# Optimization experiments

Hardware: AMD Instinct MI355X
Metric: run time of the kernel (lower is better)

Reference implementation:

```python
import jax, jax.numpy as jnp
import numpy as np

N_NODES, N_EDGES = 100000, 400000
D_NODE, D_EDGE, N_COND, N_ROUNDS = 128, 64, 2, 3


def gru_cell(x, h, Wih, Whh, bih, bhh):
    # Standard torch.nn.GRUCell math. x: [N, D] input, h: [N, D] hidden.
    gi = x @ Wih.T + bih            # [N, 3D]
    gh = h @ Whh.T + bhh            # [N, 3D]
    ir, iz, inn = jnp.split(gi, 3, axis=-1)
    hr, hz, hn = jnp.split(gh, 3, axis=-1)
    r = jax.nn.sigmoid(ir + hr)
    z = jax.nn.sigmoid(iz + hz)
    n = jnp.tanh(inn + r * hn)
    return (1.0 - z) * n + z * h


def setup_inputs() -> dict:
    key = jax.random.key(0)
    ks = jax.random.split(key, 10)
    scale = jnp.float32(0.05)
    d_in = 2 * D_NODE + D_EDGE + N_COND  # 322, matches enc_U Linear in_features
    h = jax.random.normal(ks[0], (N_NODES, D_NODE), jnp.float32)
    e = jax.random.normal(ks[1], (N_EDGES, D_EDGE), jnp.float32)
    src = jax.random.randint(ks[2], (N_EDGES,), 0, N_NODES)
    dst = jax.random.randint(ks[3], (N_EDGES,), 0, N_NODES)
    cond = jax.random.normal(ks[4], (N_COND,), jnp.float32)
    U_W = jax.random.normal(ks[5], (N_ROUNDS, D_NODE, d_in), jnp.float32) * scale
    U_b = jnp.zeros((N_ROUNDS, D_NODE), jnp.float32)
    Wih = jax.random.normal(ks[6], (N_ROUNDS, 3 * D_NODE, D_NODE), jnp.float32) * scale
    Whh = jax.random.normal(ks[7], (N_ROUNDS, 3 * D_NODE, D_NODE), jnp.float32) * scale
    bih = jnp.zeros((N_ROUNDS, 3 * D_NODE), jnp.float32)
    bhh = jnp.zeros((N_ROUNDS, 3 * D_NODE), jnp.float32)
    return dict(h=h, e=e, src=src, dst=dst, cond=cond,
                U_W=U_W, U_b=U_b, Wih=Wih, Whh=Whh, bih=bih, bhh=bhh)


def reference(h, e, src, dst, cond, U_W, U_b, Wih, Whh, bih, bhh):
    # GGM encode(): 3 rounds of gather-concat-Linear(enc_U)-segment_sum-GRUCell(enc_C).
    n_nodes = h.shape[0]
    n_edges = e.shape[0]
    cond_e = jnp.broadcast_to(cond, (n_edges, cond.shape[0]))
    for k in range(U_W.shape[0]):
        # per-edge message input: [h_v, h_w, e_vw, condition] -> [E, 2D+DE+NC]
        x = jnp.concatenate([h[dst], h[src], e, cond_e], axis=-1)
        msg = x @ U_W[k].T + U_b[k]                              # [E, D]
        agg = jax.ops.segment_sum(msg, dst, num_segments=n_nodes)  # [N, D]
        h = gru_cell(agg, h, Wih[k], Whh[k], bih[k], bhh[k])
    return h
```

## Files before the change

kernel.cpp:

```cpp
#include <hip/hip_runtime.h>
#include <hip/hip_bf16.h>
#include <hip/hip_fp16.h>


#define D_NODE 128
#define D_EDGE 64
#define D_IN   322
#define GRU3   384
#define ROWS_BLK 128
#define PA_STRIDE 328
#define PB_STRIDE 136

typedef _Float16 f16x8 __attribute__((ext_vector_type(8)));
typedef _Float16 f16x4 __attribute__((ext_vector_type(4)));
typedef _Float16 f16x2 __attribute__((ext_vector_type(2)));
typedef float    f32x4 __attribute__((ext_vector_type(4)));
typedef unsigned short u16x8 __attribute__((ext_vector_type(8)));

__device__ __forceinline__ f16x8 as_f16x8(u16x8 v) { return __builtin_bit_cast(f16x8, v); }
__device__ __forceinline__ float sigm_(float x) { return 1.f / (1.f + __expf(-x)); }
__device__ __forceinline__ float tanh_(float x) { return 1.f - 2.f / (__expf(2.f * x) + 1.f); }

__global__ void hist_k(const int* __restrict__ dst, int* __restrict__ cnt, int E) {
    int t = blockIdx.x * 256 + threadIdx.x;
    if (t < E) atomicAdd(&cnt[dst[t]], 1);
}

__global__ __launch_bounds__(256) void scan1_k(const int* __restrict__ cnt, int* __restrict__ row_ptr,
                                               int* __restrict__ blk_sums, int N) {
    __shared__ int s[256];
    const int t = threadIdx.x;
    const int base = blockIdx.x * 1024 + t * 4;
    int v0 = (base + 0 < N) ? cnt[base + 0] : 0;
    int v1 = (base + 1 < N) ? cnt[base + 1] : 0;
    int v2 = (base + 2 < N) ? cnt[base + 2] : 0;
    int v3 = (base + 3 < N) ? cnt[base + 3] : 0;
    const int tot = v0 + v1 + v2 + v3;
    s[t] = tot;
    __syncthreads();
    for (int off = 1; off < 256; off <<= 1) {
        int u = (t >= off) ? s[t - off] : 0;
        __syncthreads();
        s[t] += u;
        __syncthreads();
    }
    const int excl = s[t] - tot;
    if (base + 0 < N) row_ptr[base + 0] = excl;
    if (base + 1 < N) row_ptr[base + 1] = excl + v0;
    if (base + 2 < N) row_ptr[base + 2] = excl + v0 + v1;
    if (base + 3 < N) row_ptr[base + 3] = excl + v0 + v1 + v2;
    if (t == 255) blk_sums[blockIdx.x] = s[255];
}

__global__ __launch_bounds__(256) void scan2_k(int* __restrict__ blk_sums, int NB,
                                               int* __restrict__ row_ptr, int N, int E) {
    __shared__ int s[256];
    const int t = threadIdx.x;
    const int v = (t < NB) ? blk_sums[t] : 0;
    s[t] = v;
    __syncthreads();
    for (int off = 1; off < 256; off <<= 1) {
        int u = (t >= off) ? s[t - off] : 0;
        __syncthreads();
        s[t] += u;
        __syncthreads();
    }
    if (t < NB) blk_sums[t] = s[t] - v;
    if (t == 0) row_ptr[N] = E;
}

__global__ __launch_bounds__(256) void scan3_k(int* __restrict__ row_ptr, int* __restrict__ cursor,
                                               const int* __restrict__ blk_sums, int N) {
    const int off = blk_sums[blockIdx.x];
    const int base = blockIdx.x * 1024 + threadIdx.x * 4;
#pragma unroll
    for (int j = 0; j < 4; ++j) {
        const int i = base + j;
        if (i < N) {
            const int v = row_ptr[i] + off;
            row_ptr[i] = v;
            cursor[i] = v;
        }
    }
}

__global__ void scatter_k(const int* __restrict__ src, const int* __restrict__ dst,
                          int* __restrict__ cursor, int* __restrict__ csr_src,
                          int* __restrict__ csr_eid, int E) {
    int t = blockIdx.x * 256 + threadIdx.x;
    if (t < E) {
        int d = dst[t];
        int pos = atomicAdd(&cursor[d], 1);
        csr_src[pos] = src[t];
        csr_eid[pos] = t;
    }
}

__global__ __launch_bounds__(320) void cvt_uwp_k(const float* __restrict__ in, _Float16* __restrict__ out) {
    const int row = blockIdx.x;
    const int t = threadIdx.x;
    out[(size_t)row * 320 + t] = (_Float16)in[(size_t)row * D_IN + t];
}

__global__ void cvt_f32_k(const float* __restrict__ in, _Float16* __restrict__ out, int n) {
    int t = blockIdx.x * 256 + threadIdx.x;
    if (t < n) out[t] = (_Float16)in[t];
}

__global__ void cvt4_k(const float* __restrict__ in, _Float16* __restrict__ out, int n4) {
    int t = blockIdx.x * 256 + threadIdx.x;
    if (t < n4) {
        const f32x4 v = ((const f32x4*)in)[t];
        f16x4 r;
        r[0] = (_Float16)v[0]; r[1] = (_Float16)v[1];
        r[2] = (_Float16)v[2]; r[3] = (_Float16)v[3];
        ((f16x4*)out)[t] = r;
    }
}

__global__ void compute_c_k(const float* __restrict__ UW, const float* __restrict__ Ub,
                            const float* __restrict__ cond, float* __restrict__ cvec) {
    int t = threadIdx.x;
    if (t < 3 * D_NODE) {
        int k = t >> 7, i = t & 127;
        const float* u = UW + (size_t)k * D_NODE * D_IN + (size_t)i * D_IN + 320;
        cvec[t] = u[0] * cond[0] + u[1] * cond[1] + Ub[k * D_NODE + i];
    }
}

__global__ __launch_bounds__(256) void gather_e_k(const float* __restrict__ e,
                                                  const int* __restrict__ row_ptr,
                                                  const int* __restrict__ csr_eid,
                                                  _Float16* __restrict__ S_e, int N) {
    const int wave = threadIdx.x >> 6, lane = threadIdx.x & 63;
    const int n = blockIdx.x * 4 + wave;
    if (n >= N) return;
    const int p0 = row_ptr[n], p1 = row_ptr[n + 1];
    float a = 0.f, b = 0.f;
    int p = p0;
    for (; p + 1 < p1; p += 2) {
        const int e0 = csr_eid[p], e1 = csr_eid[p + 1];
        a += e[(size_t)e0 * D_EDGE + lane];
        b += e[(size_t)e1 * D_EDGE + lane];
    }
    if (p < p1) a += e[(size_t)csr_eid[p] * D_EDGE + lane];
    S_e[(size_t)n * D_EDGE + lane] = (_Float16)(a + b);
}

__global__ __launch_bounds__(256) void gather_h_k(const _Float16* __restrict__ h16,
                                                  const int* __restrict__ row_ptr,
                                                  const int* __restrict__ csr_src,
                                                  _Float16* __restrict__ S_h, int N) {
    const int wave = threadIdx.x >> 6, lane = threadIdx.x & 63;
    const int n = blockIdx.x * 4 + wave;
    if (n >= N) return;
    const unsigned* hp = (const unsigned*)h16;
    const int p0 = row_ptr[n], p1 = row_ptr[n + 1];
    float a0 = 0.f, a1 = 0.f, b0 = 0.f, b1 = 0.f;
    int p = p0;
    for (; p + 1 < p1; p += 2) {
        const int s0 = csr_src[p], s1 = csr_src[p + 1];
        const f16x2 v0 = __builtin_bit_cast(f16x2, hp[(size_t)s0 * 64 + lane]);
        const f16x2 v1 = __builtin_bit_cast(f16x2, hp[(size_t)s1 * 64 + lane]);
        a0 += (float)v0[0]; a1 += (float)v0[1];
        b0 += (float)v1[0]; b1 += (float)v1[1];
    }
    if (p < p1) {
        const f16x2 v = __builtin_bit_cast(f16x2, hp[(size_t)csr_src[p] * 64 + lane]);
        a0 += (float)v[0]; a1 += (float)v[1];
    }
    f16x2 r;
    r[0] = (_Float16)(a0 + b0);
    r[1] = (_Float16)(a1 + b1);
    ((unsigned*)S_h)[(size_t)n * 64 + lane] = __builtin_bit_cast(unsigned, r);
}

__global__ __launch_bounds__(256) void agg_k(
    const _Float16* __restrict__ h16,
    const _Float16* __restrict__ S_h,
    const _Float16* __restrict__ S_e,
    const int* __restrict__ row_ptr,
    const float* __restrict__ cvec,
    const _Float16* __restrict__ UWp,
    _Float16* __restrict__ agg,
    int N) {
    __shared__ __align__(16) _Float16 pbuf[2][16 * PA_STRIDE];

    const int tid  = threadIdx.x;
    const int wave = tid >> 6;
    const int lane = tid & 63;
    const int l15  = lane & 15;
    const int lg   = lane >> 4;
    const int rbase = blockIdx.x * ROWS_BLK + wave * 32;

    const unsigned short* hp  = (const unsigned short*)h16;
    const unsigned short* shp = (const unsigned short*)S_h;
    const unsigned short* sep = (const unsigned short*)S_e;
    const unsigned short* uwp = (const unsigned short*)UWp;

    f16x8 a_h[2][4], a_sh[2][4], a_se[2][2];
#pragma unroll
    for (int m = 0; m < 2; ++m) {
        const int arow = min(rbase + m * 16 + l15, N - 1);
#pragma unroll
        for (int kb = 0; kb < 4; ++kb) {
            a_h[m][kb]  = as_f16x8(*(const u16x8*)(hp  + (size_t)arow * D_NODE + kb * 32 + lg * 8));
            a_sh[m][kb] = as_f16x8(*(const u16x8*)(shp + (size_t)arow * D_NODE + kb * 32 + lg * 8));
        }
#pragma unroll
        for (int kb = 0; kb < 2; ++kb)
            a_se[m][kb] = as_f16x8(*(const u16x8*)(sep + (size_t)arow * D_EDGE + kb * 32 + lg * 8));
    }
    float degv[2][4];
#pragma unroll
    for (int m = 0; m < 2; ++m)
#pragma unroll
        for (int i = 0; i < 4; ++i) {
            const int n = min(rbase + m * 16 + lg * 4 + i, N - 1);
            degv[m][i] = (float)(row_ptr[n + 1] - row_ptr[n]);
        }

    u16x8 pr0, pr1, pr2;
    auto load_panel = [&](int nb) {
        const int c0 = tid, c1 = 256 + tid, c2 = 512 + tid;
        pr0 = *(const u16x8*)(uwp + (size_t)(nb * 16 + c0 / 40) * 320 + (c0 % 40) * 8);
        pr1 = *(const u16x8*)(uwp + (size_t)(nb * 16 + c1 / 40) * 320 + (c1 % 40) * 8);
        if (c2 < 640)
            pr2 = *(const u16x8*)(uwp + (size_t)(nb * 16 + c2 / 40) * 320 + (c2 % 40) * 8);
    };
    auto write_panel = [&](int b) {
        const int c0 = tid, c1 = 256 + tid, c2 = 512 + tid;
        *(u16x8*)&pbuf[b][(c0 / 40) * PA_STRIDE + (c0 % 40) * 8] = pr0;
        *(u16x8*)&pbuf[b][(c1 / 40) * PA_STRIDE + (c1 % 40) * 8] = pr1;
        if (c2 < 640)
            *(u16x8*)&pbuf[b][(c2 / 40) * PA_STRIDE + (c2 % 40) * 8] = pr2;
    };

    load_panel(0);
    write_panel(0);
    __syncthreads();

#pragma unroll 1
    for (int nb = 0; nb < 8; ++nb) {
        if (nb < 7) load_panel(nb + 1);
        const _Float16* bp = pbuf[nb & 1];
        f32x4 acc1[2] = {{0.f,0.f,0.f,0.f},{0.f,0.f,0.f,0.f}};
        f32x4 acc2[2] = {{0.f,0.f,0.f,0.f},{0.f,0.f,0.f,0.f}};
#pragma unroll
        for (int kb = 0; kb < 10; ++kb) {
            f16x8 b = as_f16x8(*(const u16x8*)&bp[l15 * PA_STRIDE + kb * 32 + lg * 8]);
            if (kb < 4) {
                acc1[0] = __builtin_amdgcn_mfma_f32_16x16x32_f16(a_h[0][kb], b, acc1[0], 0, 0, 0);
                acc1[1] = __builtin_amdgcn_mfma_f32_16x16x32_f16(a_h[1][kb], b, acc1[1], 0, 0, 0);
            } else if (kb < 8) {
                acc2[0] = __builtin_amdgcn_mfma_f32_16x16x32_f16(a_sh[0][kb-4], b, acc2[0], 0, 0, 0);
                acc2[1] = __builtin_amdgcn_mfma_f32_16x16x32_f16(a_sh[1][kb-4], b, acc2[1], 0, 0, 0);
            } else {
                acc2[0] = __builtin_amdgcn_mfma_f32_16x16x32_f16(a_se[0][kb-8], b, acc2[0], 0, 0, 0);
                acc2[1] = __builtin_amdgcn_mfma_f32_16x16x32_f16(a_se[1][kb-8], b, acc2[1], 0, 0, 0);
            }
        }
        const float cv = cvec[nb * 16 + l15];
#pragma unroll
        for (int m = 0; m < 2; ++m)
#pragma unroll
            for (int i = 0; i < 4; ++i) {
                const int n = rbase + m * 16 + lg * 4 + i;
                if (n < N)
                    agg[(size_t)n * D_NODE + nb * 16 + l15] =
                        (_Float16)(degv[m][i] * (acc1[m][i] + cv) + acc2[m][i]);
            }
        if (nb < 7) write_panel((nb + 1) & 1);
        __syncthreads();
    }
}

__global__ __launch_bounds__(256) void gru_k(
    const float* __restrict__ h_cur,
    _Float16* __restrict__ h16,
    const _Float16* __restrict__ agg,
    const _Float16* __restrict__ Wihh,
    const _Float16* __restrict__ Whhh,
    const float* __restrict__ bih,
    const float* __restrict__ bhh,
    float* __restrict__ h_next,
    int N) {
    __shared__ __align__(16) _Float16 pbuf[2][96 * PB_STRIDE];

    const int tid  = threadIdx.x;
    const int wave = tid >> 6;
    const int lane = tid & 63;
    const int l15  = lane & 15;
    const int lg   = lane >> 4;
    const int rbase = blockIdx.x * ROWS_BLK + wave * 32;

    const unsigned short* hp  = (const unsigned short*)h16;
    const unsigned short* agp = (const unsigned short*)agg;
    const unsigned short* wih = (const unsigned short*)Wihh;
    const unsigned short* whh = (const unsigned short*)Whhh;

    f16x8 a_ag[2][4], a_h[2][4];
#pragma unroll
    for (int m = 0; m < 2; ++m) {
        const int arow = min(rbase + m * 16 + l15, N - 1);
#pragma unroll
        for (int kb = 0; kb < 4; ++kb) {
            a_ag[m][kb] = as_f16x8(*(const u16x8*)(agp + (size_t)arow * D_NODE + kb * 32 + lg * 8));
            a_h[m][kb]  = as_f16x8(*(const u16x8*)(hp  + (size_t)arow * D_NODE + kb * 32 + lg * 8));
        }
    }

    u16x8 pr[6];
    auto load_panel = [&](int nb) {
#pragma unroll
        for (int r = 0; r < 6; ++r) {
            const int c = r * 256 + tid;
            const int row = c >> 4;
            const int off = (c & 15) * 8;
            const int gate = row >> 4;
            const int col = nb * 16 + (row & 15) + (gate % 3) * D_NODE;
            const unsigned short* mat = (gate < 3) ? wih : whh;
            pr[r] = *(const u16x8*)(mat + (size_t)col * D_NODE + off);
        }
    };
    auto write_panel = [&](int b) {
#pragma unroll
        for (int r = 0; r < 6; ++r) {
            const int c = r * 256 + tid;
            const int row = c >> 4;
            const int off = (c & 15) * 8;
            *(u16x8*)&pbuf[b][row * PB_STRIDE + off] = pr[r];
        }
    };

    load_panel(0);
    write_panel(0);
    __syncthreads();

#pragma unroll 1
    for (int nb = 0; nb < 8; ++nb) {
        if (nb < 7) load_panel(nb + 1);
        const int d = nb * 16 + l15;
        float hv[2][4];
#pragma unroll
        for (int m = 0; m < 2; ++m)
#pragma unroll
            for (int i = 0; i < 4; ++i) {
                const int n = min(rbase + m * 16 + lg * 4 + i, N - 1);
                hv[m][i] = h_cur[(size_t)n * D_NODE + d];
            }
        const float bir = bih[d],       biz = bih[128 + d], bin = bih[256 + d];
        const float bhr = bhh[d],       bhz = bhh[128 + d], bhn = bhh[256 + d];

        const _Float16* bp = pbuf[nb & 1];
        f32x4 air[2] = {{0.f,0.f,0.f,0.f},{0.f,0.f,0.f,0.f}};
        f32x4 aiz[2] = {{0.f,0.f,0.f,0.f},{0.f,0.f,0.f,0.f}};
        f32x4 ain_[2] = {{0.f,0.f,0.f,0.f},{0.f,0.f,0.f,0.f}};
        f32x4 ahr[2] = {{0.f,0.f,0.f,0.f},{0.f,0.f,0.f,0.f}};
        f32x4 ahz[2] = {{0.f,0.f,0.f,0.f},{0.f,0.f,0.f,0.f}};
        f32x4 ahn[2] = {{0.f,0.f,0.f,0.f},{0.f,0.f,0.f,0.f}};
#pragma unroll
        for (int kb = 0; kb < 4; ++kb) {
            const int ko = kb * 32 + lg * 8;
            f16x8 b;
            b = as_f16x8(*(const u16x8*)&bp[(0 * 16 + l15) * PB_STRIDE + ko]);
            air[0] = __builtin_amdgcn_mfma_f32_16x16x32_f16(a_ag[0][kb], b, air[0], 0, 0, 0);
            air[1] = __builtin_amdgcn_mfma_f32_16x16x32_f16(a_ag[1][kb], b, air[1], 0, 0, 0);
            b = as_f16x8(*(const u16x8*)&bp[(1 * 16 + l15) * PB_STRIDE + ko]);
            aiz[0] = __builtin_amdgcn_mfma_f32_16x16x32_f16(a_ag[0][kb], b, aiz[0], 0, 0, 0);
            aiz[1] = __builtin_amdgcn_mfma_f32_16x16x32_f16(a_ag[1][kb], b, aiz[1], 0, 0, 0);
            b = as_f16x8(*(const u16x8*)&bp[(2 * 16 + l15) * PB_STRIDE + ko]);
            ain_[0] = __builtin_amdgcn_mfma_f32_16x16x32_f16(a_ag[0][kb], b, ain_[0], 0, 0, 0);
            ain_[1] = __builtin_amdgcn_mfma_f32_16x16x32_f16(a_ag[1][kb], b, ain_[1], 0, 0, 0);
            b = as_f16x8(*(const u16x8*)&bp[(3 * 16 + l15) * PB_STRIDE + ko]);
            ahr[0] = __builtin_amdgcn_mfma_f32_16x16x32_f16(a_h[0][kb], b, ahr[0], 0, 0, 0);
            ahr[1] = __builtin_amdgcn_mfma_f32_16x16x32_f16(a_h[1][kb], b, ahr[1], 0, 0, 0);
            b = as_f16x8(*(const u16x8*)&bp[(4 * 16 + l15) * PB_STRIDE + ko]);
            ahz[0] = __builtin_amdgcn_mfma_f32_16x16x32_f16(a_h[0][kb], b, ahz[0], 0, 0, 0);
            ahz[1] = __builtin_amdgcn_mfma_f32_16x16x32_f16(a_h[1][kb], b, ahz[1], 0, 0, 0);
            b = as_f16x8(*(const u16x8*)&bp[(5 * 16 + l15) * PB_STRIDE + ko]);
            ahn[0] = __builtin_amdgcn_mfma_f32_16x16x32_f16(a_h[0][kb], b, ahn[0], 0, 0, 0);
            ahn[1] = __builtin_amdgcn_mfma_f32_16x16x32_f16(a_h[1][kb], b, ahn[1], 0, 0, 0);
        }
#pragma unroll
        for (int m = 0; m < 2; ++m)
#pragma unroll
            for (int i = 0; i < 4; ++i) {
                const int n = rbase + m * 16 + lg * 4 + i;
                if (n < N) {
                    const float r  = sigm_(air[m][i] + bir + ahr[m][i] + bhr);
                    const float z  = sigm_(aiz[m][i] + biz + ahz[m][i] + bhz);
                    const float nn = tanh_(ain_[m][i] + bin + r * (ahn[m][i] + bhn));
                    const float hval = (1.f - z) * nn + z * hv[m][i];
                    h_next[(size_t)n * D_NODE + d] = hval;
                    h16[(size_t)n * D_NODE + d] = (_Float16)hval;
                }
            }
        if (nb < 7) write_panel((nb + 1) & 1);
        __syncthreads();
    }
}

extern "C" void kernel_launch(void* const* d_in, const int* in_sizes, int n_in,
                              void* d_out, int out_size, void* d_ws, size_t ws_size,
                              hipStream_t stream) {
    const float* h0   = (const float*)d_in[0];
    const float* e    = (const float*)d_in[1];
    const int*   src  = (const int*)d_in[2];
    const int*   dst  = (const int*)d_in[3];
    const float* cond = (const float*)d_in[4];
    const float* UW   = (const float*)d_in[5];
    const float* Ub   = (const float*)d_in[6];
    const float* Wih  = (const float*)d_in[7];
    const float* Whh  = (const float*)d_in[8];
    const float* bih  = (const float*)d_in[9];
    const float* bhh  = (const float*)d_in[10];

    const int N = in_sizes[0] / D_NODE;
    const int E = in_sizes[2];
    const int NB = (N + 1023) / 1024;
    const int NT = (N + ROWS_BLK - 1) / ROWS_BLK;

    char* wsb = (char*)d_ws;
    size_t off = 0;
    auto carve = [&](size_t bytes) -> char* {
        char* p = wsb + off;
        off = (off + bytes + 255) & ~(size_t)255;
        return p;
    };
    int*   cnt      = (int*)carve((size_t)N * 4);
    int*   row_ptr  = (int*)carve(((size_t)N + 1) * 4);
    int*   cursor   = (int*)carve((size_t)N * 4);
    int*   csr_src  = (int*)carve((size_t)E * 4);
    int*   csr_eid  = (int*)carve((size_t)E * 4);
    int*   blk_sums = (int*)carve(256 * 4);
    float* cvec     = (float*)carve(3 * D_NODE * 4);
    _Float16* S_e  = (_Float16*)carve((size_t)N * D_EDGE * 2);
    _Float16* S_h  = (_Float16*)carve((size_t)N * D_NODE * 2);
    _Float16* aggb = (_Float16*)carve((size_t)N * D_NODE * 2);
    _Float16* h16  = (_Float16*)carve((size_t)N * D_NODE * 2);
    _Float16* UWp  = (_Float16*)carve((size_t)3 * D_NODE * 320 * 2);
    _Float16* Wihh = (_Float16*)carve((size_t)3 * GRU3 * D_NODE * 2);
    _Float16* Whhh = (_Float16*)carve((size_t)3 * GRU3 * D_NODE * 2);
    (void)ws_size; (void)n_in; (void)out_size;

    hipMemsetAsync(cnt, 0, (size_t)N * 4, stream);
    hist_k<<<(E + 255) / 256, 256, 0, stream>>>(dst, cnt, E);
    scan1_k<<<NB, 256, 0, stream>>>(cnt, row_ptr, blk_sums, N);
    scan2_k<<<1, 256, 0, stream>>>(blk_sums, NB, row_ptr, N, E);
    scan3_k<<<NB, 256, 0, stream>>>(row_ptr, cursor, blk_sums, N);
    scatter_k<<<(E + 255) / 256, 256, 0, stream>>>(src, dst, cursor, csr_src, csr_eid, E);
    compute_c_k<<<1, 384, 0, stream>>>(UW, Ub, cond, cvec);
    cvt_uwp_k<<<3 * D_NODE, 320, 0, stream>>>(UW, UWp);
    {
        const int n1 = 3 * GRU3 * D_NODE;
        cvt_f32_k<<<(n1 + 255) / 256, 256, 0, stream>>>(Wih, Wihh, n1);
        cvt_f32_k<<<(n1 + 255) / 256, 256, 0, stream>>>(Whh, Whhh, n1);
    }
    {
        const int n4 = N * D_NODE / 4;
        cvt4_k<<<(n4 + 255) / 256, 256, 0, stream>>>(h0, h16, n4);
    }
    gather_e_k<<<(N + 3) / 4, 256, 0, stream>>>(e, row_ptr, csr_eid, S_e, N);

    float* hout = (float*)d_out;
    const float* hc = h0;
    for (int k = 0; k < 3; ++k) {
        gather_h_k<<<(N + 3) / 4, 256, 0, stream>>>(h16, row_ptr, csr_src, S_h, N);
        agg_k<<<NT, 256, 0, stream>>>(
            h16, S_h, S_e, row_ptr, cvec + k * D_NODE,
            UWp + (size_t)k * D_NODE * 320, aggb, N);
        gru_k<<<NT, 256, 0, stream>>>(
            hc, h16, aggb,
            Wihh + (size_t)k * GRU3 * D_NODE,
            Whhh + (size_t)k * GRU3 * D_NODE,
            bih + (size_t)k * GRU3,
            bhh + (size_t)k * GRU3,
            hout, N);
        hc = hout;
    }
}
```

Baseline: 575.4 us.

## Carry hidden state in fp16 between rounds, unroll gathers by four, single-buffer GRU panel

The GRU kernel now reads the previous hidden state from the fp16 copy instead of the fp32 buffer, and writes the fp32 output only in the final round. This removes two fp32 hidden-state writes and the fp32 reads in every round. The gather kernels unroll by four with four independent accumulators to keep more loads in flight. The GRU weight panel goes from double to single buffering, which cuts LDS use but adds a barrier per step. The fp16 recurrence loses precision across rounds, and there is a hazard: h16 is read in place for hv while other blocks overwrite it.

```diff
diff --git a/kernel.cpp b/kernel.cpp
--- a/kernel.cpp
+++ b/kernel.cpp
@@ -136,15 +136,17 @@
     const int n = blockIdx.x * 4 + wave;
     if (n >= N) return;
     const int p0 = row_ptr[n], p1 = row_ptr[n + 1];
-    float a = 0.f, b = 0.f;
+    float a = 0.f, b = 0.f, c = 0.f, d = 0.f;
     int p = p0;
-    for (; p + 1 < p1; p += 2) {
-        const int e0 = csr_eid[p], e1 = csr_eid[p + 1];
+    for (; p + 3 < p1; p += 4) {
+        const int e0 = csr_eid[p], e1 = csr_eid[p + 1], e2 = csr_eid[p + 2], e3 = csr_eid[p + 3];
         a += e[(size_t)e0 * D_EDGE + lane];
         b += e[(size_t)e1 * D_EDGE + lane];
-    }
-    if (p < p1) a += e[(size_t)csr_eid[p] * D_EDGE + lane];
-    S_e[(size_t)n * D_EDGE + lane] = (_Float16)(a + b);
+        c += e[(size_t)e2 * D_EDGE + lane];
+        d += e[(size_t)e3 * D_EDGE + lane];
+    }
+    for (; p < p1; ++p) a += e[(size_t)csr_eid[p] * D_EDGE + lane];
+    S_e[(size_t)n * D_EDGE + lane] = (_Float16)((a + b) + (c + d));
 }
 
 __global__ __launch_bounds__(256) void gather_h_k(const _Float16* __restrict__ h16,
@@ -157,21 +159,26 @@
     const unsigned* hp = (const unsigned*)h16;
     const int p0 = row_ptr[n], p1 = row_ptr[n + 1];
     float a0 = 0.f, a1 = 0.f, b0 = 0.f, b1 = 0.f;
+    float c0 = 0.f, c1 = 0.f, d0 = 0.f, d1 = 0.f;
     int p = p0;
-    for (; p + 1 < p1; p += 2) {
-        const int s0 = csr_src[p], s1 = csr_src[p + 1];
+    for (; p + 3 < p1; p += 4) {
+        const int s0 = csr_src[p], s1 = csr_src[p + 1], s2 = csr_src[p + 2], s3 = csr_src[p + 3];
         const f16x2 v0 = __builtin_bit_cast(f16x2, hp[(size_t)s0 * 64 + lane]);
         const f16x2 v1 = __builtin_bit_cast(f16x2, hp[(size_t)s1 * 64 + lane]);
+        const f16x2 v2 = __builtin_bit_cast(f16x2, hp[(size_t)s2 * 64 + lane]);
+        const f16x2 v3 = __builtin_bit_cast(f16x2, hp[(size_t)s3 * 64 + lane]);
         a0 += (float)v0[0]; a1 += (float)v0[1];
         b0 += (float)v1[0]; b1 += (float)v1[1];
-    }
-    if (p < p1) {
+        c0 += (float)v2[0]; c1 += (float)v2[1];
+        d0 += (float)v3[0]; d1 += (float)v3[1];
+    }
+    for (; p < p1; ++p) {
         const f16x2 v = __builtin_bit_cast(f16x2, hp[(size_t)csr_src[p] * 64 + lane]);
         a0 += (float)v[0]; a1 += (float)v[1];
     }
     f16x2 r;
-    r[0] = (_Float16)(a0 + b0);
-    r[1] = (_Float16)(a1 + b1);
+    r[0] = (_Float16)((a0 + b0) + (c0 + d0));
+    r[1] = (_Float16)((a1 + b1) + (c1 + d1));
     ((unsigned*)S_h)[(size_t)n * 64 + lane] = __builtin_bit_cast(unsigned, r);
 }
 
@@ -276,7 +283,6 @@
 }
 
 __global__ __launch_bounds__(256) void gru_k(
-    const float* __restrict__ h_cur,
     _Float16* __restrict__ h16,
     const _Float16* __restrict__ agg,
     const _Float16* __restrict__ Wihh,
@@ -284,8 +290,8 @@
     const float* __restrict__ bih,
     const float* __restrict__ bhh,
     float* __restrict__ h_next,
-    int N) {
-    __shared__ __align__(16) _Float16 pbuf[2][96 * PB_STRIDE];
+    int write_f32, int N) {
+    __shared__ __align__(16) _Float16 pbuf[96 * PB_STRIDE];
 
     const int tid  = threadIdx.x;
     const int wave = tid >> 6;
@@ -323,18 +329,18 @@
             pr[r] = *(const u16x8*)(mat + (size_t)col * D_NODE + off);
         }
     };
-    auto write_panel = [&](int b) {
+    auto write_panel = [&]() {
 #pragma unroll
         for (int r = 0; r < 6; ++r) {
             const int c = r * 256 + tid;
             const int row = c >> 4;
             const int off = (c & 15) * 8;
-            *(u16x8*)&pbuf[b][row * PB_STRIDE + off] = pr[r];
+            *(u16x8*)&pbuf[row * PB_STRIDE + off] = pr[r];
         }
     };
 
     load_panel(0);
-    write_panel(0);
+    write_panel();
     __syncthreads();
 
 #pragma unroll 1
@@ -347,12 +353,11 @@
 #pragma unroll
             for (int i = 0; i < 4; ++i) {
                 const int n = min(rbase + m * 16 + lg * 4 + i, N - 1);
-                hv[m][i] = h_cur[(size_t)n * D_NODE + d];
+                hv[m][i] = (float)h16[(size_t)n * D_NODE + d];
             }
         const float bir = bih[d],       biz = bih[128 + d], bin = bih[256 + d];
         const float bhr = bhh[d],       bhz = bhh[128 + d], bhn = bhh[256 + d];
 
-        const _Float16* bp = pbuf[nb & 1];
         f32x4 air[2] = {{0.f,0.f,0.f,0.f},{0.f,0.f,0.f,0.f}};
         f32x4 aiz[2] = {{0.f,0.f,0.f,0.f},{0.f,0.f,0.f,0.f}};
         f32x4 ain_[2] = {{0.f,0.f,0.f,0.f},{0.f,0.f,0.f,0.f}};
@@ -363,22 +368,22 @@
         for (int kb = 0; kb < 4; ++kb) {
             const int ko = kb * 32 + lg * 8;
             f16x8 b;
-            b = as_f16x8(*(const u16x8*)&bp[(0 * 16 + l15) * PB_STRIDE + ko]);
+            b = as_f16x8(*(const u16x8*)&pbuf[(0 * 16 + l15) * PB_STRIDE + ko]);
             air[0] = __builtin_amdgcn_mfma_f32_16x16x32_f16(a_ag[0][kb], b, air[0], 0, 0, 0);
             air[1] = __builtin_amdgcn_mfma_f32_16x16x32_f16(a_ag[1][kb], b, air[1], 0, 0, 0);
-            b = as_f16x8(*(const u16x8*)&bp[(1 * 16 + l15) * PB_STRIDE + ko]);
+            b = as_f16x8(*(const u16x8*)&pbuf[(1 * 16 + l15) * PB_STRIDE + ko]);
             aiz[0] = __builtin_amdgcn_mfma_f32_16x16x32_f16(a_ag[0][kb], b, aiz[0], 0, 0, 0);
             aiz[1] = __builtin_amdgcn_mfma_f32_16x16x32_f16(a_ag[1][kb], b, aiz[1], 0, 0, 0);
-            b = as_f16x8(*(const u16x8*)&bp[(2 * 16 + l15) * PB_STRIDE + ko]);
+            b = as_f16x8(*(const u16x8*)&pbuf[(2 * 16 + l15) * PB_STRIDE + ko]);
             ain_[0] = __builtin_amdgcn_mfma_f32_16x16x32_f16(a_ag[0][kb], b, ain_[0], 0, 0, 0);
             ain_[1] = __builtin_amdgcn_mfma_f32_16x16x32_f16(a_ag[1][kb], b, ain_[1], 0, 0, 0);
-            b = as_f16x8(*(const u16x8*)&bp[(3 * 16 + l15) * PB_STRIDE + ko]);
+            b = as_f16x8(*(const u16x8*)&pbuf[(3 * 16 + l15) * PB_STRIDE + ko]);
             ahr[0] = __builtin_amdgcn_mfma_f32_16x16x32_f16(a_h[0][kb], b, ahr[0], 0, 0, 0);
             ahr[1] = __builtin_amdgcn_mfma_f32_16x16x32_f16(a_h[1][kb], b, ahr[1], 0, 0, 0);
-            b = as_f16x8(*(const u16x8*)&bp[(4 * 16 + l15) * PB_STRIDE + ko]);
+            b = as_f16x8(*(const u16x8*)&pbuf[(4 * 16 + l15) * PB_STRIDE + ko]);
             ahz[0] = __builtin_amdgcn_mfma_f32_16x16x32_f16(a_h[0][kb], b, ahz[0], 0, 0, 0);
             ahz[1] = __builtin_amdgcn_mfma_f32_16x16x32_f16(a_h[1][kb], b, ahz[1], 0, 0, 0);
-            b = as_f16x8(*(const u16x8*)&bp[(5 * 16 + l15) * PB_STRIDE + ko]);
+            b = as_f16x8(*(const u16x8*)&pbuf[(5 * 16 + l15) * PB_STRIDE + ko]);
             ahn[0] = __builtin_amdgcn_mfma_f32_16x16x32_f16(a_h[0][kb], b, ahn[0], 0, 0, 0);
             ahn[1] = __builtin_amdgcn_mfma_f32_16x16x32_f16(a_h[1][kb], b, ahn[1], 0, 0, 0);
         }
@@ -392,12 +397,15 @@
                     const float z  = sigm_(aiz[m][i] + biz + ahz[m][i] + bhz);
                     const float nn = tanh_(ain_[m][i] + bin + r * (ahn[m][i] + bhn));
                     const float hval = (1.f - z) * nn + z * hv[m][i];
-                    h_next[(size_t)n * D_NODE + d] = hval;
+                    if (write_f32) h_next[(size_t)n * D_NODE + d] = hval;
                     h16[(size_t)n * D_NODE + d] = (_Float16)hval;
                 }
             }
-        if (nb < 7) write_panel((nb + 1) & 1);
-        __syncthreads();
+        if (nb < 7) {
+            __syncthreads();
+            write_panel();
+            __syncthreads();
+        }
     }
 }
 
@@ -464,19 +472,17 @@
     gather_e_k<<<(N + 3) / 4, 256, 0, stream>>>(e, row_ptr, csr_eid, S_e, N);
 
     float* hout = (float*)d_out;
-    const float* hc = h0;
     for (int k = 0; k < 3; ++k) {
         gather_h_k<<<(N + 3) / 4, 256, 0, stream>>>(h16, row_ptr, csr_src, S_h, N);
         agg_k<<<NT, 256, 0, stream>>>(
             h16, S_h, S_e, row_ptr, cvec + k * D_NODE,
             UWp + (size_t)k * D_NODE * 320, aggb, N);
         gru_k<<<NT, 256, 0, stream>>>(
-            hc, h16, aggb,
+            h16, aggb,
             Wihh + (size_t)k * GRU3 * D_NODE,
             Whhh + (size_t)k * GRU3 * D_NODE,
             bih + (size_t)k * GRU3,
             bhh + (size_t)k * GRU3,
-            hout, N);
-        hc = hout;
-    }
-}
+            hout, (k == 2) ? 1 : 0, N);
+    }
+}
```

New measurement: 679.1 us. 1.18x slower.
